# Kernel optimization log

Hardware: AMD Instinct MI355X
Metric: run time of the kernel (lower is better)

## Reference

```python
import jax, jax.numpy as jnp
import numpy as np

DIM = 4096
N_HEADS = 32
N_KV_HEADS = 8
HEAD_DIM = DIM // N_HEADS
N_REP = N_HEADS // N_KV_HEADS
SEQ_LEN = 2048
ROPE_THETA = 10000.0


def rope_cos_sin(head_dim, seq_len, theta):
    freqs = 1.0 / (theta ** (jnp.arange(0, head_dim, 2, dtype=jnp.float32) / head_dim))  # [hd/2]
    t = jnp.arange(seq_len, dtype=jnp.float32)
    angles = jnp.outer(t, freqs)  # [S, hd/2]
    return jnp.cos(angles), jnp.sin(angles)


def apply_rope(x, cos, sin):
    # x: [B, S, H, hd]; complex rotation on interleaved (even, odd) pairs
    xr = x[..., 0::2].astype(jnp.float32)
    xi = x[..., 1::2].astype(jnp.float32)
    c = cos[None, :, None, :]
    s = sin[None, :, None, :]
    out_r = xr * c - xi * s
    out_i = xr * s + xi * c
    out = jnp.stack([out_r, out_i], axis=-1).reshape(x.shape)
    return out.astype(x.dtype)


def setup_inputs() -> dict:
    key = jax.random.key(0)
    ks = jax.random.split(key, 5)
    x = jax.random.normal(ks[0], (1, SEQ_LEN, DIM), dtype=jnp.float32)
    wq = jax.random.normal(ks[1], (DIM, DIM), dtype=jnp.float32) * (DIM ** -0.5)
    wk = jax.random.normal(ks[2], (N_KV_HEADS * HEAD_DIM, DIM), dtype=jnp.float32) * (DIM ** -0.5)
    wv = jax.random.normal(ks[3], (N_KV_HEADS * HEAD_DIM, DIM), dtype=jnp.float32) * (DIM ** -0.5)
    wo = jax.random.normal(ks[4], (DIM, DIM), dtype=jnp.float32) * (DIM ** -0.5)
    return {"x": x, "start_pos": 0, "wq": wq, "wk": wk, "wv": wv, "wo": wo}


def reference(x, start_pos, wq, wk, wv, wo):
    bsz, seq_len, _ = x.shape
    # projections (torch Linear: y = x @ W.T)
    xq = (x @ wq.T).reshape(bsz, seq_len, N_HEADS, HEAD_DIM)
    xk = (x @ wk.T).reshape(bsz, seq_len, N_KV_HEADS, HEAD_DIM)
    xv = (x @ wv.T).reshape(bsz, seq_len, N_KV_HEADS, HEAD_DIM)

    cos, sin = rope_cos_sin(HEAD_DIM, seq_len, ROPE_THETA)
    xq = apply_rope(xq, cos, sin)
    xk = apply_rope(xk, cos, sin)

    # repeat_kv (GQA): [B, S, Hkv, hd] -> [B, S, Hkv*n_rep, hd]
    keys = jnp.repeat(xk, N_REP, axis=2)
    values = jnp.repeat(xv, N_REP, axis=2)

    # [B, H, S, hd]
    q = xq.transpose(0, 2, 1, 3)
    k = keys.transpose(0, 2, 1, 3)
    v = values.transpose(0, 2, 1, 3)

    scale = 1.0 / jnp.sqrt(jnp.asarray(HEAD_DIM, dtype=jnp.float32))
    scores = jnp.einsum('bhqd,bhkd->bhqk', q, k) * scale  # [B, H, S, S]
    causal = jnp.tril(jnp.ones((seq_len, seq_len), dtype=bool))
    scores = jnp.where(causal[None, None], scores, -jnp.inf)
    attn = jax.nn.softmax(scores.astype(jnp.float32), axis=-1).astype(q.dtype)
    out = jnp.einsum('bhqk,bhkd->bhqd', attn, v)  # [B, H, S, hd]
    out = out.transpose(0, 2, 1, 3).reshape(bsz, seq_len, -1)
    return out @ wo.T
```

## Files before the change

kernel.cpp:

```cpp
#include <hip/hip_runtime.h>

#define DIM 4096
#define KVDIM 1024
#define KVSTRIDE 2048
#define SEQ 2048
#define HEADS 32
#define HD 128

typedef __attribute__((ext_vector_type(8))) short bf16x8;
typedef __attribute__((ext_vector_type(4))) float f32x4;
typedef __attribute__((ext_vector_type(16))) float f32x16;
typedef __attribute__((ext_vector_type(4))) int int4v;

__device__ inline unsigned short f2bf(float f) {
    union { float f; unsigned int u; } v; v.f = f;
    unsigned int r = v.u + 0x7fffu + ((v.u >> 16) & 1u);
    return (unsigned short)(r >> 16);
}
__device__ inline float bf2f(unsigned short h) {
    union { unsigned int u; float f; } v; v.u = ((unsigned int)h) << 16;
    return v.f;
}

__device__ inline void gld16(const void* g, void* l) {
    __builtin_amdgcn_global_load_lds(
        (const __attribute__((address_space(1))) void*)g,
        (__attribute__((address_space(3))) void*)l, 16, 0, 0);
}

__device__ inline unsigned cvtpk(float a, float b) {
    unsigned r;
    asm("v_cvt_pk_bf16_f32 %0, %1, %2" : "=v"(r) : "v"(a), "v"(b));
    return r;
}

__global__ void convert_f32_bf16(const float* __restrict__ in,
                                 unsigned short* __restrict__ out, int n) {
    int i = (blockIdx.x * blockDim.x + threadIdx.x) * 8;
    if (i >= n) return;
    const float4* p = (const float4*)(in + i);
    float4 a = p[0], b = p[1];
    bf16x8 o;
    o[0] = (short)f2bf(a.x); o[1] = (short)f2bf(a.y);
    o[2] = (short)f2bf(a.z); o[3] = (short)f2bf(a.w);
    o[4] = (short)f2bf(b.x); o[5] = (short)f2bf(b.y);
    o[6] = (short)f2bf(b.z); o[7] = (short)f2bf(b.w);
    *(bf16x8*)(out + i) = o;
}

__global__ void rope_table(float* __restrict__ cs, float* __restrict__ sn) {
    int i = blockIdx.x * blockDim.x + threadIdx.x;
    if (i >= SEQ * 64) return;
    int m = i >> 6, f = i & 63;
    float freq = expf(-(float)f * (9.210340371976184f / 64.0f));
    float ang = (float)m * freq;
    float s, c;
    sincosf(ang, &s, &c);
    cs[i] = c; sn[i] = s;
}

__global__ void rope_apply(unsigned short* __restrict__ q, int lppr, int stride, float scale,
                           const float* __restrict__ cs, const float* __restrict__ sn) {
    int i = blockIdx.x * blockDim.x + threadIdx.x;
    int m = i >> lppr;
    int p = i & ((1 << lppr) - 1);
    if (m >= SEQ) return;
    int f = p & 63;
    int col = ((p >> 6) << 7) + (f << 1);
    size_t idx = (size_t)m * stride + col;
    unsigned int u = *(const unsigned int*)&q[idx];
    float xr = bf2f((unsigned short)(u & 0xffffu));
    float xi = bf2f((unsigned short)(u >> 16));
    float c = cs[(m << 6) + f], s = sn[(m << 6) + f];
    float orr = (xr * c - xi * s) * scale;
    float oi  = (xr * s + xi * c) * scale;
    unsigned int w = ((unsigned int)f2bf(oi) << 16) | (unsigned int)f2bf(orr);
    *(unsigned int*)&q[idx] = w;
}

template <bool OUT_BF16>
__global__ __launch_bounds__(256)
void gemm_bt(const unsigned short* __restrict__ A,
             const unsigned short* __restrict__ W,
             void* __restrict__ Cout, int M, int N, int K) {
    __shared__ __align__(16) unsigned short As[128 * 64];
    __shared__ __align__(16) unsigned short Ws[128 * 64];

    int nwg = gridDim.x * gridDim.y;
    int wg = blockIdx.y * gridDim.x + blockIdx.x;
    int cpx = nwg >> 3;
    wg = (wg & 7) * cpx + (wg >> 3);
    int bx = wg % gridDim.x, by = wg / gridDim.x;
    int brow = by * 128, bcol = bx * 128;

    int tid = threadIdx.x, lane = tid & 63, wid = tid >> 6;
    int wr = wid >> 1, wc = wid & 1, l15 = lane & 15, lq = lane >> 4;

    f32x4 acc[4][4] = {};

    for (int bk = 0; bk < K; bk += 64) {
        #pragma unroll
        for (int it = 0; it < 4; ++it) {
            int slot = it * 256 + wid * 64 + lane;
            int r = slot >> 3, g = slot & 7;
            gld16(&A[(size_t)(brow + r) * K + bk + ((g ^ (r & 7)) << 3)],
                  &As[(it * 256 + wid * 64) * 8]);
        }
        #pragma unroll
        for (int it = 0; it < 4; ++it) {
            int slot = it * 256 + wid * 64 + lane;
            int r = slot >> 3, g = slot & 7;
            gld16(&W[(size_t)(bcol + r) * K + bk + ((g ^ (r & 7)) << 3)],
                  &Ws[(it * 256 + wid * 64) * 8]);
        }
        __syncthreads();

        #pragma unroll
        for (int kk = 0; kk < 64; kk += 32) {
            int gb = (kk >> 3) + lq;
            bf16x8 af[4], bfr[4];
            #pragma unroll
            for (int m = 0; m < 4; ++m) {
                int r = wr * 64 + m * 16 + l15;
                af[m] = *(const bf16x8*)&As[r * 64 + ((gb ^ (r & 7)) << 3)];
            }
            #pragma unroll
            for (int n = 0; n < 4; ++n) {
                int r = wc * 64 + n * 16 + l15;
                bfr[n] = *(const bf16x8*)&Ws[r * 64 + ((gb ^ (r & 7)) << 3)];
            }
            #pragma unroll
            for (int m = 0; m < 4; ++m)
                #pragma unroll
                for (int n = 0; n < 4; ++n)
                    acc[m][n] = __builtin_amdgcn_mfma_f32_16x16x32_bf16(
                        af[m], bfr[n], acc[m][n], 0, 0, 0);
        }
        __syncthreads();
    }

    #pragma unroll
    for (int m = 0; m < 4; ++m) {
        #pragma unroll
        for (int n = 0; n < 4; ++n) {
            int row0 = brow + wr * 64 + m * 16 + lq * 4;
            int col = bcol + wc * 64 + n * 16 + l15;
            #pragma unroll
            for (int r = 0; r < 4; ++r) {
                if (OUT_BF16)
                    ((unsigned short*)Cout)[(size_t)(row0 + r) * N + col] = f2bf(acc[m][n][r]);
                else
                    ((float*)Cout)[(size_t)(row0 + r) * N + col] = acc[m][n][r];
            }
        }
    }
}

__global__ __launch_bounds__(256)
void attn_kernel(const unsigned short* __restrict__ Q,
                 const unsigned short* __restrict__ KV,
                 unsigned short* __restrict__ O) {
    __shared__ __align__(16) unsigned short ks[64 * 128];
    __shared__ __align__(16) unsigned short vt[128][66];

    int h = blockIdx.x;
    int yy = (gridDim.y - 1) - blockIdx.y;
    int q0 = yy * 128;
    int kvh = h >> 2;
    int tid = threadIdx.x, lane = tid & 63, wid = tid >> 6;
    int l31 = lane & 31, l5 = lane >> 5;
    int qw0 = q0 + wid * 32;

    bf16x8 qf[8];
    #pragma unroll
    for (int k8 = 0; k8 < 8; ++k8)
        qf[k8] = *(const bf16x8*)&Q[(size_t)(qw0 + l31) * DIM + h * HD + k8 * 16 + l5 * 8];

    f32x16 o_acc[4] = {};
    float m_run = -1e30f, l_run = 0.0f;

    int k4 = tid >> 4;
    int d0 = (tid & 15) * 8;

    int ntiles = (q0 + 128) >> 6;
    for (int t = 0; t < ntiles; ++t) {
        int kv0 = t * 64;
        #pragma unroll
        for (int it = 0; it < 4; ++it) {
            int slot = it * 256 + wid * 64 + lane;
            int r = slot >> 4, g = slot & 15;
            gld16(&KV[(size_t)(kv0 + r) * KVSTRIDE + kvh * HD + ((g ^ (r & 7)) << 3)],
                  &ks[(it * 256 + wid * 64) * 8]);
        }
        {
            bf16x8 v0 = *(const bf16x8*)&KV[(size_t)(kv0 + k4 * 4 + 0) * KVSTRIDE + KVDIM + kvh * HD + d0];
            bf16x8 v1 = *(const bf16x8*)&KV[(size_t)(kv0 + k4 * 4 + 1) * KVSTRIDE + KVDIM + kvh * HD + d0];
            bf16x8 v2 = *(const bf16x8*)&KV[(size_t)(kv0 + k4 * 4 + 2) * KVSTRIDE + KVDIM + kvh * HD + d0];
            bf16x8 v3 = *(const bf16x8*)&KV[(size_t)(kv0 + k4 * 4 + 3) * KVSTRIDE + KVDIM + kvh * HD + d0];
            #pragma unroll
            for (int j = 0; j < 8; ++j) {
                unsigned lo = ((unsigned)(unsigned short)v1[j] << 16) | (unsigned)(unsigned short)v0[j];
                unsigned hi = ((unsigned)(unsigned short)v3[j] << 16) | (unsigned)(unsigned short)v2[j];
                *(unsigned*)&vt[d0 + j][k4 * 4]     = lo;
                *(unsigned*)&vt[d0 + j][k4 * 4 + 2] = hi;
            }
        }
        __syncthreads();

        if (kv0 <= qw0 + 31) {
            #pragma unroll
            for (int sub = 0; sub < 2; ++sub) {
                int kvs = kv0 + sub * 32;
                if (kvs > qw0 + 31) continue;
                f32x16 s = {};
                #pragma unroll
                for (int k8 = 0; k8 < 8; ++k8) {
                    int r = sub * 32 + l31;
                    bf16x8 kf = *(const bf16x8*)&ks[r * 128 + (((k8 * 2 + l5) ^ (r & 7)) << 3)];
                    s = __builtin_amdgcn_mfma_f32_32x32x16_bf16(kf, qf[k8], s, 0, 0, 0);
                }
                if (kvs + 31 > qw0) {
                    #pragma unroll
                    for (int r = 0; r < 16; ++r) {
                        int kv = kvs + (r & 3) + ((r >> 2) << 3) + l5 * 4;
                        if (kv > qw0 + l31) s[r] = -1e30f;
                    }
                }
                float mx = s[0];
                #pragma unroll
                for (int r = 1; r < 16; ++r) mx = fmaxf(mx, s[r]);
                mx = fmaxf(mx, __shfl_xor(mx, 32));
                bool need = mx > m_run + 8.0f;
                if (__any((int)need)) {
                    float mn = fmaxf(m_run, mx);
                    float al = exp2f(m_run - mn);
                    m_run = mn;
                    l_run *= al;
                    #pragma unroll
                    for (int r = 0; r < 16; ++r) {
                        int qlr = (r & 3) + ((r >> 2) << 3) + l5 * 4;
                        float alO = __shfl(al, qlr, 32);
                        #pragma unroll
                        for (int t32 = 0; t32 < 4; ++t32) o_acc[t32][r] *= alO;
                    }
                }
                #pragma unroll
                for (int r = 0; r < 16; ++r) {
                    float p = exp2f(s[r] - m_run);
                    l_run += p;
                    s[r] = p;
                }
                bf16x8 pa[2];
                #pragma unroll
                for (int kk1 = 0; kk1 < 2; ++kk1) {
                    unsigned u0 = cvtpk(s[kk1 * 8 + 0], s[kk1 * 8 + 1]);
                    unsigned u1 = cvtpk(s[kk1 * 8 + 2], s[kk1 * 8 + 3]);
                    unsigned u2 = cvtpk(s[kk1 * 8 + 4], s[kk1 * 8 + 5]);
                    unsigned u3 = cvtpk(s[kk1 * 8 + 6], s[kk1 * 8 + 7]);
                    unsigned t0 = (unsigned)__shfl_xor((int)(l5 ? u0 : u2), 32);
                    unsigned t1 = (unsigned)__shfl_xor((int)(l5 ? u1 : u3), 32);
                    int4v w;
                    w.x = (int)(l5 ? t0 : u0);
                    w.y = (int)(l5 ? t1 : u1);
                    w.z = (int)(l5 ? u2 : t0);
                    w.w = (int)(l5 ? u3 : t1);
                    pa[kk1] = __builtin_bit_cast(bf16x8, w);
                }
                #pragma unroll
                for (int t32 = 0; t32 < 4; ++t32) {
                    #pragma unroll
                    for (int kk1 = 0; kk1 < 2; ++kk1) {
                        const unsigned short* vrow =
                            &vt[t32 * 32 + l31][sub * 32 + kk1 * 16 + l5 * 8];
                        int4v w;
                        w.x = *(const int*)&vrow[0];
                        w.y = *(const int*)&vrow[2];
                        w.z = *(const int*)&vrow[4];
                        w.w = *(const int*)&vrow[6];
                        o_acc[t32] = __builtin_amdgcn_mfma_f32_32x32x16_bf16(
                            pa[kk1], __builtin_bit_cast(bf16x8, w), o_acc[t32], 0, 0, 0);
                    }
                }
            }
        }
        __syncthreads();
    }

    float l_tot = l_run + __shfl_xor(l_run, 32);
    float rinv = __builtin_amdgcn_rcpf(l_tot);
    #pragma unroll
    for (int r = 0; r < 16; ++r) {
        int qlr = (r & 3) + ((r >> 2) << 3) + l5 * 4;
        float rl = __shfl(rinv, qlr, 32);
        #pragma unroll
        for (int t32 = 0; t32 < 4; ++t32)
            O[(size_t)(qw0 + qlr) * DIM + h * HD + t32 * 32 + l31] =
                f2bf(o_acc[t32][r] * rl);
    }
}

extern "C" void kernel_launch(void* const* d_in, const int* in_sizes, int n_in,
                              void* d_out, int out_size, void* d_ws, size_t ws_size,
                              hipStream_t stream) {
    const float* x  = (const float*)d_in[0];
    const float* wq = (const float*)d_in[2];
    const float* wk = (const float*)d_in[3];
    const float* wv = (const float*)d_in[4];
    const float* wo = (const float*)d_in[5];
    float* out = (float*)d_out;

    char* ws = (char*)d_ws;
    unsigned short* xb  = (unsigned short*)(ws);
    unsigned short* qb  = (unsigned short*)(ws + 16777216);
    unsigned short* kvb = (unsigned short*)(ws + 33554432);
    unsigned short* ab  = (unsigned short*)(ws + 41943040);
    float* cs = (float*)(ws + 58720256);
    float* sn = cs + SEQ * 64;
    unsigned short* wscratch = (unsigned short*)d_out;
    unsigned short* wob = (unsigned short*)(ws);

    const float SCALE2 = 0.08838834764831845f * 1.4426950408889634f;

    convert_f32_bf16<<<SEQ * DIM / 2048, 256, 0, stream>>>(x, xb, SEQ * DIM);
    rope_table<<<SEQ * 64 / 256, 256, 0, stream>>>(cs, sn);

    convert_f32_bf16<<<DIM * DIM / 2048, 256, 0, stream>>>(wq, wscratch, DIM * DIM);
    gemm_bt<true><<<dim3(DIM / 128, SEQ / 128), 256, 0, stream>>>(xb, wscratch, qb, SEQ, DIM, DIM);

    convert_f32_bf16<<<KVDIM * DIM / 2048, 256, 0, stream>>>(wk, wscratch, KVDIM * DIM);
    convert_f32_bf16<<<KVDIM * DIM / 2048, 256, 0, stream>>>(wv, wscratch + (size_t)KVDIM * DIM, KVDIM * DIM);
    gemm_bt<true><<<dim3(KVSTRIDE / 128, SEQ / 128), 256, 0, stream>>>(xb, wscratch, kvb, SEQ, KVSTRIDE, DIM);

    rope_apply<<<SEQ * (DIM / 2) / 256, 256, 0, stream>>>(qb, 11, DIM, SCALE2, cs, sn);
    rope_apply<<<SEQ * (KVDIM / 2) / 256, 256, 0, stream>>>(kvb, 9, KVSTRIDE, 1.0f, cs, sn);

    attn_kernel<<<dim3(HEADS, SEQ / 128), 256, 0, stream>>>(qb, kvb, ab);

    convert_f32_bf16<<<DIM * DIM / 2048, 256, 0, stream>>>(wo, wob, DIM * DIM);
    gemm_bt<false><<<dim3(DIM / 128, SEQ / 128), 256, 0, stream>>>(ab, wob, out, SEQ, DIM, DIM);
}
```

Before: 397.9 us.

## Split attention KV range across two wave groups and merge partial softmax

The attention kernel now runs 512 threads per block. Two groups of four waves each process alternating 64-row KV tiles for the same 128 query rows, and their partial max, sum and output are merged through shared memory at the end. The V transpose buffer now uses an XOR-swizzled layout so each MFMA operand is read with one 128-bit LDS load, and s_setprio is raised around the MFMA sections. The aim is more waves per CU and shorter serial KV loops. The cost is an extra merge step, a bf16 rounding of the partial output, and more LDS per block.

```diff
diff --git a/kernel.cpp b/kernel.cpp
--- a/kernel.cpp
+++ b/kernel.cpp
@@ -156,20 +156,77 @@
     }
 }
 
-__global__ __launch_bounds__(256)
+
+__device__ __forceinline__ void softmax_pack(
+    f32x16& s, f32x16* o_acc, float& m_run, float& l_run,
+    int qw0, int kvs, int l31, int l5, bf16x8* pa) {
+    if (kvs + 31 > qw0) {
+        #pragma unroll
+        for (int r = 0; r < 16; ++r) {
+            int kv = kvs + (r & 3) + ((r >> 2) << 3) + l5 * 4;
+            if (kv > qw0 + l31) s[r] = -1e30f;
+        }
+    }
+    float mx = s[0];
+    #pragma unroll
+    for (int r = 1; r < 16; ++r) mx = fmaxf(mx, s[r]);
+    mx = fmaxf(mx, __shfl_xor(mx, 32));
+    bool need = mx > m_run + 8.0f;
+    if (__any((int)need)) {
+        float mn = fmaxf(m_run, mx);
+        float al = exp2f(m_run - mn);
+        m_run = mn;
+        l_run *= al;
+        #pragma unroll
+        for (int r = 0; r < 16; ++r) {
+            int qlr = (r & 3) + ((r >> 2) << 3) + l5 * 4;
+            float alO = __shfl(al, qlr, 32);
+            #pragma unroll
+            for (int t32 = 0; t32 < 4; ++t32) o_acc[t32][r] *= alO;
+        }
+    }
+    #pragma unroll
+    for (int r = 0; r < 16; ++r) {
+        float p = exp2f(s[r] - m_run);
+        l_run += p;
+        s[r] = p;
+    }
+    #pragma unroll
+    for (int kk1 = 0; kk1 < 2; ++kk1) {
+        unsigned u0 = cvtpk(s[kk1 * 8 + 0], s[kk1 * 8 + 1]);
+        unsigned u1 = cvtpk(s[kk1 * 8 + 2], s[kk1 * 8 + 3]);
+        unsigned u2 = cvtpk(s[kk1 * 8 + 4], s[kk1 * 8 + 5]);
+        unsigned u3 = cvtpk(s[kk1 * 8 + 6], s[kk1 * 8 + 7]);
+        unsigned t0 = (unsigned)__shfl_xor((int)(l5 ? u0 : u2), 32);
+        unsigned t1 = (unsigned)__shfl_xor((int)(l5 ? u1 : u3), 32);
+        int4v w;
+        w.x = (int)(l5 ? t0 : u0);
+        w.y = (int)(l5 ? t1 : u1);
+        w.z = (int)(l5 ? u2 : t0);
+        w.w = (int)(l5 ? u3 : t1);
+        pa[kk1] = __builtin_bit_cast(bf16x8, w);
+    }
+}
+
+__global__ __launch_bounds__(512, 4)
 void attn_kernel(const unsigned short* __restrict__ Q,
                  const unsigned short* __restrict__ KV,
                  unsigned short* __restrict__ O) {
-    __shared__ __align__(16) unsigned short ks[64 * 128];
-    __shared__ __align__(16) unsigned short vt[128][66];
+    __shared__ __align__(16) unsigned short smem[32768];
+
+    unsigned short* ks0 = smem;
+    unsigned short* ks1 = smem + 8192;
+    unsigned short* vt0 = smem + 16384;
+    unsigned short* vt1 = smem + 24576;
 
     int h = blockIdx.x;
     int yy = (gridDim.y - 1) - blockIdx.y;
     int q0 = yy * 128;
     int kvh = h >> 2;
     int tid = threadIdx.x, lane = tid & 63, wid = tid >> 6;
+    int qsub = wid & 3, half = wid >> 2;
     int l31 = lane & 31, l5 = lane >> 5;
-    int qw0 = q0 + wid * 32;
+    int qw0 = q0 + qsub * 32;
 
     bf16x8 qf[8];
     #pragma unroll
@@ -179,123 +236,122 @@
     f32x16 o_acc[4] = {};
     float m_run = -1e30f, l_run = 0.0f;
 
-    int k4 = tid >> 4;
+    int k2 = tid >> 4;
     int d0 = (tid & 15) * 8;
-
-    int ntiles = (q0 + 128) >> 6;
-    for (int t = 0; t < ntiles; ++t) {
-        int kv0 = t * 64;
-        #pragma unroll
-        for (int it = 0; it < 4; ++it) {
-            int slot = it * 256 + wid * 64 + lane;
-            int r = slot >> 4, g = slot & 15;
-            gld16(&KV[(size_t)(kv0 + r) * KVSTRIDE + kvh * HD + ((g ^ (r & 7)) << 3)],
-                  &ks[(it * 256 + wid * 64) * 8]);
-        }
-        {
-            bf16x8 v0 = *(const bf16x8*)&KV[(size_t)(kv0 + k4 * 4 + 0) * KVSTRIDE + KVDIM + kvh * HD + d0];
-            bf16x8 v1 = *(const bf16x8*)&KV[(size_t)(kv0 + k4 * 4 + 1) * KVSTRIDE + KVDIM + kvh * HD + d0];
-            bf16x8 v2 = *(const bf16x8*)&KV[(size_t)(kv0 + k4 * 4 + 2) * KVSTRIDE + KVDIM + kvh * HD + d0];
-            bf16x8 v3 = *(const bf16x8*)&KV[(size_t)(kv0 + k4 * 4 + 3) * KVSTRIDE + KVDIM + kvh * HD + d0];
+    int vsub = (k2 & 3) * 2;
+    int vg = k2 >> 2;
+
+    const unsigned short* Kb = KV + kvh * HD;
+    const unsigned short* Vb = KV + KVDIM + kvh * HD;
+
+    unsigned short* myks = half ? ks1 : ks0;
+    unsigned short* myvt = half ? vt1 : vt0;
+
+    int np = yy + 1;
+    for (int i = 0; i < np; ++i) {
+        #pragma unroll
+        for (int tt = 0; tt < 2; ++tt) {
+            int kvb = (2 * i + tt) * 64;
+            unsigned short* kd = tt ? ks1 : ks0;
+            #pragma unroll
+            for (int it = 0; it < 2; ++it) {
+                int slot = it * 512 + tid;
+                int r = slot >> 4, g = slot & 15;
+                gld16(&Kb[(size_t)(kvb + r) * KVSTRIDE + ((g ^ (r & 7)) << 3)],
+                      &kd[(it * 512 + wid * 64) * 8]);
+            }
+        }
+        #pragma unroll
+        for (int tt = 0; tt < 2; ++tt) {
+            int kvb = (2 * i + tt) * 64;
+            unsigned short* vd = tt ? vt1 : vt0;
+            bf16x8 va = *(const bf16x8*)&Vb[(size_t)(kvb + k2 * 2) * KVSTRIDE + d0];
+            bf16x8 vb = *(const bf16x8*)&Vb[(size_t)(kvb + k2 * 2 + 1) * KVSTRIDE + d0];
             #pragma unroll
             for (int j = 0; j < 8; ++j) {
-                unsigned lo = ((unsigned)(unsigned short)v1[j] << 16) | (unsigned)(unsigned short)v0[j];
-                unsigned hi = ((unsigned)(unsigned short)v3[j] << 16) | (unsigned)(unsigned short)v2[j];
-                *(unsigned*)&vt[d0 + j][k4 * 4]     = lo;
-                *(unsigned*)&vt[d0 + j][k4 * 4 + 2] = hi;
+                int row = d0 + j;
+                int swz = ((row >> 3) ^ row) & 7;
+                unsigned w = ((unsigned)(unsigned short)vb[j] << 16) |
+                             (unsigned)(unsigned short)va[j];
+                *(unsigned*)&vd[row * 64 + ((vg ^ swz) << 3) + vsub] = w;
             }
         }
         __syncthreads();
 
+        int kv0 = (2 * i + half) * 64;
         if (kv0 <= qw0 + 31) {
             #pragma unroll
             for (int sub = 0; sub < 2; ++sub) {
                 int kvs = kv0 + sub * 32;
                 if (kvs > qw0 + 31) continue;
                 f32x16 s = {};
+                __builtin_amdgcn_s_setprio(1);
                 #pragma unroll
                 for (int k8 = 0; k8 < 8; ++k8) {
                     int r = sub * 32 + l31;
-                    bf16x8 kf = *(const bf16x8*)&ks[r * 128 + (((k8 * 2 + l5) ^ (r & 7)) << 3)];
+                    bf16x8 kf = *(const bf16x8*)&myks[r * 128 + (((k8 * 2 + l5) ^ (r & 7)) << 3)];
                     s = __builtin_amdgcn_mfma_f32_32x32x16_bf16(kf, qf[k8], s, 0, 0, 0);
                 }
-                if (kvs + 31 > qw0) {
-                    #pragma unroll
-                    for (int r = 0; r < 16; ++r) {
-                        int kv = kvs + (r & 3) + ((r >> 2) << 3) + l5 * 4;
-                        if (kv > qw0 + l31) s[r] = -1e30f;
-                    }
-                }
-                float mx = s[0];
-                #pragma unroll
-                for (int r = 1; r < 16; ++r) mx = fmaxf(mx, s[r]);
-                mx = fmaxf(mx, __shfl_xor(mx, 32));
-                bool need = mx > m_run + 8.0f;
-                if (__any((int)need)) {
-                    float mn = fmaxf(m_run, mx);
-                    float al = exp2f(m_run - mn);
-                    m_run = mn;
-                    l_run *= al;
-                    #pragma unroll
-                    for (int r = 0; r < 16; ++r) {
-                        int qlr = (r & 3) + ((r >> 2) << 3) + l5 * 4;
-                        float alO = __shfl(al, qlr, 32);
-                        #pragma unroll
-                        for (int t32 = 0; t32 < 4; ++t32) o_acc[t32][r] *= alO;
-                    }
-                }
-                #pragma unroll
-                for (int r = 0; r < 16; ++r) {
-                    float p = exp2f(s[r] - m_run);
-                    l_run += p;
-                    s[r] = p;
-                }
+                __builtin_amdgcn_s_setprio(0);
                 bf16x8 pa[2];
-                #pragma unroll
-                for (int kk1 = 0; kk1 < 2; ++kk1) {
-                    unsigned u0 = cvtpk(s[kk1 * 8 + 0], s[kk1 * 8 + 1]);
-                    unsigned u1 = cvtpk(s[kk1 * 8 + 2], s[kk1 * 8 + 3]);
-                    unsigned u2 = cvtpk(s[kk1 * 8 + 4], s[kk1 * 8 + 5]);
-                    unsigned u3 = cvtpk(s[kk1 * 8 + 6], s[kk1 * 8 + 7]);
-                    unsigned t0 = (unsigned)__shfl_xor((int)(l5 ? u0 : u2), 32);
-                    unsigned t1 = (unsigned)__shfl_xor((int)(l5 ? u1 : u3), 32);
-                    int4v w;
-                    w.x = (int)(l5 ? t0 : u0);
-                    w.y = (int)(l5 ? t1 : u1);
-                    w.z = (int)(l5 ? u2 : t0);
-                    w.w = (int)(l5 ? u3 : t1);
-                    pa[kk1] = __builtin_bit_cast(bf16x8, w);
-                }
+                softmax_pack(s, o_acc, m_run, l_run, qw0, kvs, l31, l5, pa);
+                __builtin_amdgcn_s_setprio(1);
                 #pragma unroll
                 for (int t32 = 0; t32 < 4; ++t32) {
+                    int d = t32 * 32 + l31;
+                    int swz = ((d >> 3) ^ d) & 7;
                     #pragma unroll
                     for (int kk1 = 0; kk1 < 2; ++kk1) {
-                        const unsigned short* vrow =
-                            &vt[t32 * 32 + l31][sub * 32 + kk1 * 16 + l5 * 8];
-                        int4v w;
-                        w.x = *(const int*)&vrow[0];
-                        w.y = *(const int*)&vrow[2];
-                        w.z = *(const int*)&vrow[4];
-                        w.w = *(const int*)&vrow[6];
+                        int g = sub * 4 + kk1 * 2 + l5;
+                        int4v w = *(const int4v*)&myvt[d * 64 + ((g ^ swz) << 3)];
                         o_acc[t32] = __builtin_amdgcn_mfma_f32_32x32x16_bf16(
                             pa[kk1], __builtin_bit_cast(bf16x8, w), o_acc[t32], 0, 0, 0);
                     }
                 }
+                __builtin_amdgcn_s_setprio(0);
             }
         }
         __syncthreads();
     }
 
-    float l_tot = l_run + __shfl_xor(l_run, 32);
-    float rinv = __builtin_amdgcn_rcpf(l_tot);
-    #pragma unroll
-    for (int r = 0; r < 16; ++r) {
-        int qlr = (r & 3) + ((r >> 2) << 3) + l5 * 4;
-        float rl = __shfl(rinv, qlr, 32);
-        #pragma unroll
-        for (int t32 = 0; t32 < 4; ++t32)
-            O[(size_t)(qw0 + qlr) * DIM + h * HD + t32 * 32 + l31] =
-                f2bf(o_acc[t32][r] * rl);
+    float* part_m = (float*)smem;
+    float* part_l = (float*)(smem + 512);
+    unsigned* part_o = (unsigned*)(smem + 1024);
+
+    if (half == 1) {
+        part_m[qsub * 64 + lane] = m_run;
+        part_l[qsub * 64 + lane] = l_run;
+        #pragma unroll
+        for (int t32 = 0; t32 < 4; ++t32) {
+            unsigned* po = &part_o[((qsub * 4 + t32) * 64 + lane) * 8];
+            #pragma unroll
+            for (int p = 0; p < 8; ++p)
+                po[p] = cvtpk(o_acc[t32][2 * p], o_acc[t32][2 * p + 1]);
+        }
+    }
+    __syncthreads();
+    if (half == 0) {
+        float m1 = part_m[qsub * 64 + lane];
+        float l1 = part_l[qsub * 64 + lane];
+        float mm = fmaxf(m_run, m1);
+        float a0 = exp2f(m_run - mm), a1 = exp2f(m1 - mm);
+        float lm = l_run * a0 + l1 * a1;
+        float l_tot = lm + __shfl_xor(lm, 32);
+        float rinv = __builtin_amdgcn_rcpf(l_tot);
+        #pragma unroll
+        for (int r = 0; r < 16; ++r) {
+            int qlr = (r & 3) + ((r >> 2) << 3) + l5 * 4;
+            float A0 = __shfl(a0, qlr, 32);
+            float A1 = __shfl(a1, qlr, 32);
+            float rl = __shfl(rinv, qlr, 32);
+            #pragma unroll
+            for (int t32 = 0; t32 < 4; ++t32) {
+                unsigned u = part_o[((qsub * 4 + t32) * 64 + lane) * 8 + (r >> 1)];
+                float o1 = bf2f((unsigned short)((r & 1) ? (u >> 16) : (u & 0xffffu)));
+                float om = o_acc[t32][r] * A0 + o1 * A1;
+                O[(size_t)(qw0 + qlr) * DIM + h * HD + t32 * 32 + l31] = f2bf(om * rl);
+            }
+        }
     }
 }
 
@@ -334,7 +390,7 @@
     rope_apply<<<SEQ * (DIM / 2) / 256, 256, 0, stream>>>(qb, 11, DIM, SCALE2, cs, sn);
     rope_apply<<<SEQ * (KVDIM / 2) / 256, 256, 0, stream>>>(kvb, 9, KVSTRIDE, 1.0f, cs, sn);
 
-    attn_kernel<<<dim3(HEADS, SEQ / 128), 256, 0, stream>>>(qb, kvb, ab);
+    attn_kernel<<<dim3(HEADS, 16), 512, 0, stream>>>(qb, kvb, ab);
 
     convert_f32_bf16<<<DIM * DIM / 2048, 256, 0, stream>>>(wo, wob, DIM * DIM);
     gemm_bt<false><<<dim3(DIM / 128, SEQ / 128), 256, 0, stream>>>(ab, wob, out, SEQ, DIM, DIM);
```

Result: slower. 469.4 us (+18.0%).

## Split causal attention KV range in two halves and merge partial results

Applied to the files above, without the earlier changes.

The attention grid doubles so that each 128-query block's KV tiles are split evenly between two workgroups. This targets the causal load imbalance and the low block count of the previous launch. Each half writes an unnormalized bf16 partial output plus per-row max and sum, and a new merge kernel rescales and combines them. The change also swizzles the transposed V layout in LDS so each read is a single 16-byte access, adds s_setprio around the MFMA sections, and sets a launch-bounds occupancy hint. The cost is an extra kernel pass over the output and extra rounding from storing unnormalized partials in bf16.

```diff
diff --git a/kernel.cpp b/kernel.cpp
--- a/kernel.cpp
+++ b/kernel.cpp
@@ -156,15 +156,71 @@
     }
 }
 
-__global__ __launch_bounds__(256)
+
+__device__ __forceinline__ void softmax_pack(
+    f32x16& s, f32x16* o_acc, float& m_run, float& l_run,
+    int qw0, int kvs, int l31, int l5, bf16x8* pa) {
+    if (kvs + 31 > qw0) {
+        #pragma unroll
+        for (int r = 0; r < 16; ++r) {
+            int kv = kvs + (r & 3) + ((r >> 2) << 3) + l5 * 4;
+            if (kv > qw0 + l31) s[r] = -1e30f;
+        }
+    }
+    float mx = s[0];
+    #pragma unroll
+    for (int r = 1; r < 16; ++r) mx = fmaxf(mx, s[r]);
+    mx = fmaxf(mx, __shfl_xor(mx, 32));
+    bool need = mx > m_run + 8.0f;
+    if (__any((int)need)) {
+        float mn = fmaxf(m_run, mx);
+        float al = exp2f(m_run - mn);
+        m_run = mn;
+        l_run *= al;
+        #pragma unroll
+        for (int r = 0; r < 16; ++r) {
+            int qlr = (r & 3) + ((r >> 2) << 3) + l5 * 4;
+            float alO = __shfl(al, qlr, 32);
+            #pragma unroll
+            for (int t32 = 0; t32 < 4; ++t32) o_acc[t32][r] *= alO;
+        }
+    }
+    #pragma unroll
+    for (int r = 0; r < 16; ++r) {
+        float p = exp2f(s[r] - m_run);
+        l_run += p;
+        s[r] = p;
+    }
+    #pragma unroll
+    for (int kk1 = 0; kk1 < 2; ++kk1) {
+        unsigned u0 = cvtpk(s[kk1 * 8 + 0], s[kk1 * 8 + 1]);
+        unsigned u1 = cvtpk(s[kk1 * 8 + 2], s[kk1 * 8 + 3]);
+        unsigned u2 = cvtpk(s[kk1 * 8 + 4], s[kk1 * 8 + 5]);
+        unsigned u3 = cvtpk(s[kk1 * 8 + 6], s[kk1 * 8 + 7]);
+        unsigned t0 = (unsigned)__shfl_xor((int)(l5 ? u0 : u2), 32);
+        unsigned t1 = (unsigned)__shfl_xor((int)(l5 ? u1 : u3), 32);
+        int4v w;
+        w.x = (int)(l5 ? t0 : u0);
+        w.y = (int)(l5 ? t1 : u1);
+        w.z = (int)(l5 ? u2 : t0);
+        w.w = (int)(l5 ? u3 : t1);
+        pa[kk1] = __builtin_bit_cast(bf16x8, w);
+    }
+}
+
+__global__ __launch_bounds__(256, 4)
 void attn_kernel(const unsigned short* __restrict__ Q,
                  const unsigned short* __restrict__ KV,
-                 unsigned short* __restrict__ O) {
+                 unsigned short* __restrict__ pO0,
+                 unsigned short* __restrict__ pO1,
+                 float2* __restrict__ ml) {
     __shared__ __align__(16) unsigned short ks[64 * 128];
-    __shared__ __align__(16) unsigned short vt[128][66];
+    __shared__ __align__(16) unsigned short vt[128 * 64];
 
     int h = blockIdx.x;
-    int yy = (gridDim.y - 1) - blockIdx.y;
+    int by = blockIdx.y;
+    int yy = 15 - (by >> 1);
+    int half = by & 1;
     int q0 = yy * 128;
     int kvh = h >> 2;
     int tid = threadIdx.x, lane = tid & 63, wid = tid >> 6;
@@ -181,28 +237,33 @@
 
     int k4 = tid >> 4;
     int d0 = (tid & 15) * 8;
-
-    int ntiles = (q0 + 128) >> 6;
-    for (int t = 0; t < ntiles; ++t) {
+    int vsub = (k4 & 1) * 4;
+    int vg = k4 >> 1;
+
+    const unsigned short* Kb = KV + kvh * HD;
+    const unsigned short* Vb = KV + KVDIM + kvh * HD;
+
+    int t0 = half * (yy + 1), t1 = t0 + (yy + 1);
+    for (int t = t0; t < t1; ++t) {
         int kv0 = t * 64;
         #pragma unroll
         for (int it = 0; it < 4; ++it) {
             int slot = it * 256 + wid * 64 + lane;
             int r = slot >> 4, g = slot & 15;
-            gld16(&KV[(size_t)(kv0 + r) * KVSTRIDE + kvh * HD + ((g ^ (r & 7)) << 3)],
+            gld16(&Kb[(size_t)(kv0 + r) * KVSTRIDE + ((g ^ (r & 7)) << 3)],
                   &ks[(it * 256 + wid * 64) * 8]);
         }
-        {
-            bf16x8 v0 = *(const bf16x8*)&KV[(size_t)(kv0 + k4 * 4 + 0) * KVSTRIDE + KVDIM + kvh * HD + d0];
-            bf16x8 v1 = *(const bf16x8*)&KV[(size_t)(kv0 + k4 * 4 + 1) * KVSTRIDE + KVDIM + kvh * HD + d0];
-            bf16x8 v2 = *(const bf16x8*)&KV[(size_t)(kv0 + k4 * 4 + 2) * KVSTRIDE + KVDIM + kvh * HD + d0];
-            bf16x8 v3 = *(const bf16x8*)&KV[(size_t)(kv0 + k4 * 4 + 3) * KVSTRIDE + KVDIM + kvh * HD + d0];
+        #pragma unroll
+        for (int pass = 0; pass < 2; ++pass) {
+            bf16x8 va = *(const bf16x8*)&Vb[(size_t)(kv0 + k4 * 4 + pass * 2) * KVSTRIDE + d0];
+            bf16x8 vb = *(const bf16x8*)&Vb[(size_t)(kv0 + k4 * 4 + pass * 2 + 1) * KVSTRIDE + d0];
             #pragma unroll
             for (int j = 0; j < 8; ++j) {
-                unsigned lo = ((unsigned)(unsigned short)v1[j] << 16) | (unsigned)(unsigned short)v0[j];
-                unsigned hi = ((unsigned)(unsigned short)v3[j] << 16) | (unsigned)(unsigned short)v2[j];
-                *(unsigned*)&vt[d0 + j][k4 * 4]     = lo;
-                *(unsigned*)&vt[d0 + j][k4 * 4 + 2] = hi;
+                int row = d0 + j;
+                int swz = ((row >> 3) ^ row) & 7;
+                unsigned w = ((unsigned)(unsigned short)vb[j] << 16) |
+                             (unsigned)(unsigned short)va[j];
+                *(unsigned*)&vt[row * 64 + ((vg ^ swz) << 3) + vsub + pass * 2] = w;
             }
         }
         __syncthreads();
@@ -213,90 +274,72 @@
                 int kvs = kv0 + sub * 32;
                 if (kvs > qw0 + 31) continue;
                 f32x16 s = {};
+                __builtin_amdgcn_s_setprio(1);
                 #pragma unroll
                 for (int k8 = 0; k8 < 8; ++k8) {
                     int r = sub * 32 + l31;
                     bf16x8 kf = *(const bf16x8*)&ks[r * 128 + (((k8 * 2 + l5) ^ (r & 7)) << 3)];
                     s = __builtin_amdgcn_mfma_f32_32x32x16_bf16(kf, qf[k8], s, 0, 0, 0);
                 }
-                if (kvs + 31 > qw0) {
-                    #pragma unroll
-                    for (int r = 0; r < 16; ++r) {
-                        int kv = kvs + (r & 3) + ((r >> 2) << 3) + l5 * 4;
-                        if (kv > qw0 + l31) s[r] = -1e30f;
-                    }
-                }
-                float mx = s[0];
-                #pragma unroll
-                for (int r = 1; r < 16; ++r) mx = fmaxf(mx, s[r]);
-                mx = fmaxf(mx, __shfl_xor(mx, 32));
-                bool need = mx > m_run + 8.0f;
-                if (__any((int)need)) {
-                    float mn = fmaxf(m_run, mx);
-                    float al = exp2f(m_run - mn);
-                    m_run = mn;
-                    l_run *= al;
-                    #pragma unroll
-                    for (int r = 0; r < 16; ++r) {
-                        int qlr = (r & 3) + ((r >> 2) << 3) + l5 * 4;
-                        float alO = __shfl(al, qlr, 32);
-                        #pragma unroll
-                        for (int t32 = 0; t32 < 4; ++t32) o_acc[t32][r] *= alO;
-                    }
-                }
-                #pragma unroll
-                for (int r = 0; r < 16; ++r) {
-                    float p = exp2f(s[r] - m_run);
-                    l_run += p;
-                    s[r] = p;
-                }
+                __builtin_amdgcn_s_setprio(0);
                 bf16x8 pa[2];
-                #pragma unroll
-                for (int kk1 = 0; kk1 < 2; ++kk1) {
-                    unsigned u0 = cvtpk(s[kk1 * 8 + 0], s[kk1 * 8 + 1]);
-                    unsigned u1 = cvtpk(s[kk1 * 8 + 2], s[kk1 * 8 + 3]);
-                    unsigned u2 = cvtpk(s[kk1 * 8 + 4], s[kk1 * 8 + 5]);
-                    unsigned u3 = cvtpk(s[kk1 * 8 + 6], s[kk1 * 8 + 7]);
-                    unsigned t0 = (unsigned)__shfl_xor((int)(l5 ? u0 : u2), 32);
-                    unsigned t1 = (unsigned)__shfl_xor((int)(l5 ? u1 : u3), 32);
-                    int4v w;
-                    w.x = (int)(l5 ? t0 : u0);
-                    w.y = (int)(l5 ? t1 : u1);
-                    w.z = (int)(l5 ? u2 : t0);
-                    w.w = (int)(l5 ? u3 : t1);
-                    pa[kk1] = __builtin_bit_cast(bf16x8, w);
-                }
+                softmax_pack(s, o_acc, m_run, l_run, qw0, kvs, l31, l5, pa);
+                __builtin_amdgcn_s_setprio(1);
                 #pragma unroll
                 for (int t32 = 0; t32 < 4; ++t32) {
+                    int d = t32 * 32 + l31;
+                    int swz = ((d >> 3) ^ d) & 7;
                     #pragma unroll
                     for (int kk1 = 0; kk1 < 2; ++kk1) {
-                        const unsigned short* vrow =
-                            &vt[t32 * 32 + l31][sub * 32 + kk1 * 16 + l5 * 8];
-                        int4v w;
-                        w.x = *(const int*)&vrow[0];
-                        w.y = *(const int*)&vrow[2];
-                        w.z = *(const int*)&vrow[4];
-                        w.w = *(const int*)&vrow[6];
+                        int g = sub * 4 + kk1 * 2 + l5;
+                        int4v w = *(const int4v*)&vt[d * 64 + ((g ^ swz) << 3)];
                         o_acc[t32] = __builtin_amdgcn_mfma_f32_32x32x16_bf16(
                             pa[kk1], __builtin_bit_cast(bf16x8, w), o_acc[t32], 0, 0, 0);
                     }
                 }
+                __builtin_amdgcn_s_setprio(0);
             }
         }
         __syncthreads();
     }
 
-    float l_tot = l_run + __shfl_xor(l_run, 32);
-    float rinv = __builtin_amdgcn_rcpf(l_tot);
+    float l_half = l_run + __shfl_xor(l_run, 32);
+    if (l5 == 0) {
+        float2 v; v.x = m_run; v.y = l_half;
+        ml[((size_t)(half << 11) + qw0 + l31) * 32 + h] = v;
+    }
+    unsigned short* pO = half ? pO1 : pO0;
     #pragma unroll
     for (int r = 0; r < 16; ++r) {
         int qlr = (r & 3) + ((r >> 2) << 3) + l5 * 4;
-        float rl = __shfl(rinv, qlr, 32);
         #pragma unroll
         for (int t32 = 0; t32 < 4; ++t32)
-            O[(size_t)(qw0 + qlr) * DIM + h * HD + t32 * 32 + l31] =
-                f2bf(o_acc[t32][r] * rl);
-    }
+            pO[(size_t)(qw0 + qlr) * DIM + h * HD + t32 * 32 + l31] =
+                f2bf(o_acc[t32][r]);
+    }
+}
+
+__global__ void attn_merge(const unsigned short* __restrict__ pO0,
+                           unsigned short* __restrict__ pO1out,
+                           const float2* __restrict__ ml) {
+    int i = blockIdx.x * blockDim.x + threadIdx.x;
+    int base = i * 8;
+    if (base >= SEQ * DIM) return;
+    int row = base >> 12;
+    int h = (base & 4095) >> 7;
+    float2 ml0 = ml[(size_t)row * 32 + h];
+    float2 ml1 = ml[(size_t)(2048 + row) * 32 + h];
+    float mm = fmaxf(ml0.x, ml1.x);
+    float a0 = exp2f(ml0.x - mm), a1 = exp2f(ml1.x - mm);
+    float rinv = __builtin_amdgcn_rcpf(ml0.y * a0 + ml1.y * a1);
+    bf16x8 o0 = *(const bf16x8*)&pO0[base];
+    bf16x8 o1 = *(const bf16x8*)&pO1out[base];
+    bf16x8 o;
+    #pragma unroll
+    for (int j = 0; j < 8; ++j)
+        o[j] = (short)f2bf((bf2f((unsigned short)o0[j]) * a0 +
+                            bf2f((unsigned short)o1[j]) * a1) * rinv);
+    *(bf16x8*)&pO1out[base] = o;
 }
 
 extern "C" void kernel_launch(void* const* d_in, const int* in_sizes, int n_in,
@@ -316,6 +359,7 @@
     unsigned short* ab  = (unsigned short*)(ws + 41943040);
     float* cs = (float*)(ws + 58720256);
     float* sn = cs + SEQ * 64;
+    float2* ml = (float2*)(ws + 58720256);
     unsigned short* wscratch = (unsigned short*)d_out;
     unsigned short* wob = (unsigned short*)(ws);
 
@@ -334,7 +378,8 @@
     rope_apply<<<SEQ * (DIM / 2) / 256, 256, 0, stream>>>(qb, 11, DIM, SCALE2, cs, sn);
     rope_apply<<<SEQ * (KVDIM / 2) / 256, 256, 0, stream>>>(kvb, 9, KVSTRIDE, 1.0f, cs, sn);
 
-    attn_kernel<<<dim3(HEADS, SEQ / 128), 256, 0, stream>>>(qb, kvb, ab);
+    attn_kernel<<<dim3(HEADS, 32), 256, 0, stream>>>(qb, kvb, xb, ab, ml);
+    attn_merge<<<SEQ * DIM / 8 / 256, 256, 0, stream>>>(xb, ab, ml);
 
     convert_f32_bf16<<<DIM * DIM / 2048, 256, 0, stream>>>(wo, wob, DIM * DIM);
     gemm_bt<false><<<dim3(DIM / 128, SEQ / 128), 256, 0, stream>>>(ab, wob, out, SEQ, DIM, DIM);
```

Result: slower. 550.4 us (+38.3%).

## Fuse Q and KV projections into one GEMM with RoPE in epilogue

Applied to the files above, without the earlier changes.

Merges the separate Q and KV projection GEMMs into a single launch over a 48x16 grid, where column blocks select the Q or KV weight. RoPE and the softmax scale are applied in the GEMM epilogue using a lane shuffle to pair even and odd columns, which removes the two rope_apply passes over Q and K. The fused launch should also fill the GPU better than two separate grids did. In exchange, the epilogue does extra table loads and shuffles, and the KV weights are staged in the attention output buffer.

```diff
diff --git a/kernel.cpp b/kernel.cpp
--- a/kernel.cpp
+++ b/kernel.cpp
@@ -6,6 +6,7 @@
 #define SEQ 2048
 #define HEADS 32
 #define HD 128
+#define SCALE2F 0.12753785016058262f
 
 typedef __attribute__((ext_vector_type(8))) short bf16x8;
 typedef __attribute__((ext_vector_type(4))) float f32x4;
@@ -59,25 +60,6 @@
     cs[i] = c; sn[i] = s;
 }
 
-__global__ void rope_apply(unsigned short* __restrict__ q, int lppr, int stride, float scale,
-                           const float* __restrict__ cs, const float* __restrict__ sn) {
-    int i = blockIdx.x * blockDim.x + threadIdx.x;
-    int m = i >> lppr;
-    int p = i & ((1 << lppr) - 1);
-    if (m >= SEQ) return;
-    int f = p & 63;
-    int col = ((p >> 6) << 7) + (f << 1);
-    size_t idx = (size_t)m * stride + col;
-    unsigned int u = *(const unsigned int*)&q[idx];
-    float xr = bf2f((unsigned short)(u & 0xffffu));
-    float xi = bf2f((unsigned short)(u >> 16));
-    float c = cs[(m << 6) + f], s = sn[(m << 6) + f];
-    float orr = (xr * c - xi * s) * scale;
-    float oi  = (xr * s + xi * c) * scale;
-    unsigned int w = ((unsigned int)f2bf(oi) << 16) | (unsigned int)f2bf(orr);
-    *(unsigned int*)&q[idx] = w;
-}
-
 template <bool OUT_BF16>
 __global__ __launch_bounds__(256)
 void gemm_bt(const unsigned short* __restrict__ A,
@@ -151,6 +133,105 @@
                     ((unsigned short*)Cout)[(size_t)(row0 + r) * N + col] = f2bf(acc[m][n][r]);
                 else
                     ((float*)Cout)[(size_t)(row0 + r) * N + col] = acc[m][n][r];
+            }
+        }
+    }
+}
+
+__global__ __launch_bounds__(256)
+void gemm_qkv(const unsigned short* __restrict__ A,
+              const unsigned short* __restrict__ Wq,
+              const unsigned short* __restrict__ Wkv,
+              unsigned short* __restrict__ Qout,
+              unsigned short* __restrict__ KVout,
+              const float* __restrict__ cs, const float* __restrict__ sn) {
+    __shared__ __align__(16) unsigned short As[128 * 64];
+    __shared__ __align__(16) unsigned short Ws[128 * 64];
+    const int K = DIM;
+
+    int nwg = gridDim.x * gridDim.y;
+    int wg = blockIdx.y * gridDim.x + blockIdx.x;
+    int cpx = nwg >> 3;
+    wg = (wg & 7) * cpx + (wg >> 3);
+    int bx = wg % gridDim.x, by = wg / gridDim.x;
+    int brow = by * 128, bcol = bx * 128;
+
+    bool isQ = bx < 32;
+    const unsigned short* Wb = isQ ? Wq : Wkv;
+    int wrow0 = isQ ? bcol : bcol - 4096;
+
+    int tid = threadIdx.x, lane = tid & 63, wid = tid >> 6;
+    int wr = wid >> 1, wc = wid & 1, l15 = lane & 15, lq = lane >> 4;
+
+    f32x4 acc[4][4] = {};
+
+    for (int bk = 0; bk < K; bk += 64) {
+        #pragma unroll
+        for (int it = 0; it < 4; ++it) {
+            int slot = it * 256 + wid * 64 + lane;
+            int r = slot >> 3, g = slot & 7;
+            gld16(&A[(size_t)(brow + r) * K + bk + ((g ^ (r & 7)) << 3)],
+                  &As[(it * 256 + wid * 64) * 8]);
+        }
+        #pragma unroll
+        for (int it = 0; it < 4; ++it) {
+            int slot = it * 256 + wid * 64 + lane;
+            int r = slot >> 3, g = slot & 7;
+            gld16(&Wb[(size_t)(wrow0 + r) * K + bk + ((g ^ (r & 7)) << 3)],
+                  &Ws[(it * 256 + wid * 64) * 8]);
+        }
+        __syncthreads();
+
+        #pragma unroll
+        for (int kk = 0; kk < 64; kk += 32) {
+            int gb = (kk >> 3) + lq;
+            bf16x8 af[4], bfr[4];
+            #pragma unroll
+            for (int m = 0; m < 4; ++m) {
+                int r = wr * 64 + m * 16 + l15;
+                af[m] = *(const bf16x8*)&As[r * 64 + ((gb ^ (r & 7)) << 3)];
+            }
+            #pragma unroll
+            for (int n = 0; n < 4; ++n) {
+                int r = wc * 64 + n * 16 + l15;
+                bfr[n] = *(const bf16x8*)&Ws[r * 64 + ((gb ^ (r & 7)) << 3)];
+            }
+            #pragma unroll
+            for (int m = 0; m < 4; ++m)
+                #pragma unroll
+                for (int n = 0; n < 4; ++n)
+                    acc[m][n] = __builtin_amdgcn_mfma_f32_16x16x32_bf16(
+                        af[m], bfr[n], acc[m][n], 0, 0, 0);
+        }
+        __syncthreads();
+    }
+
+    bool dorope = bx < 40;
+    float scl = isQ ? SCALE2F : 1.0f;
+    unsigned short* outp = isQ ? Qout : KVout;
+    int ostride = isQ ? DIM : KVSTRIDE;
+    int ocol0 = wrow0 + wc * 64;
+    bool evenlane = (l15 & 1) == 0;
+
+    #pragma unroll
+    for (int m = 0; m < 4; ++m) {
+        #pragma unroll
+        for (int n = 0; n < 4; ++n) {
+            int col = ocol0 + n * 16 + l15;
+            int f = (col & 127) >> 1;
+            int row0 = brow + wr * 64 + m * 16 + lq * 4;
+            #pragma unroll
+            for (int r = 0; r < 4; ++r) {
+                float v = acc[m][n][r];
+                if (dorope) {
+                    float p = __shfl_xor(v, 1);
+                    int ti = ((row0 + r) << 6) + f;
+                    float c = cs[ti], s = sn[ti];
+                    float xr = evenlane ? v : p;
+                    float xi = evenlane ? p : v;
+                    v = (evenlane ? (xr * c - xi * s) : (xr * s + xi * c)) * scl;
+                }
+                outp[(size_t)(row0 + r) * ostride + col] = f2bf(v);
             }
         }
     }
@@ -310,29 +391,24 @@
     float* out = (float*)d_out;
 
     char* ws = (char*)d_ws;
-    unsigned short* xb  = (unsigned short*)(ws);
-    unsigned short* qb  = (unsigned short*)(ws + 16777216);
-    unsigned short* kvb = (unsigned short*)(ws + 33554432);
-    unsigned short* ab  = (unsigned short*)(ws + 41943040);
+    unsigned short* xb   = (unsigned short*)(ws);
+    unsigned short* qb   = (unsigned short*)(ws + 16777216);
+    unsigned short* kvb  = (unsigned short*)(ws + 33554432);
+    unsigned short* ab   = (unsigned short*)(ws + 41943040);
     float* cs = (float*)(ws + 58720256);
     float* sn = cs + SEQ * 64;
-    unsigned short* wscratch = (unsigned short*)d_out;
-    unsigned short* wob = (unsigned short*)(ws);
-
-    const float SCALE2 = 0.08838834764831845f * 1.4426950408889634f;
+    unsigned short* wqb  = (unsigned short*)d_out;
+    unsigned short* wkvb = ab;
+    unsigned short* wob  = (unsigned short*)(ws);
 
     convert_f32_bf16<<<SEQ * DIM / 2048, 256, 0, stream>>>(x, xb, SEQ * DIM);
     rope_table<<<SEQ * 64 / 256, 256, 0, stream>>>(cs, sn);
 
-    convert_f32_bf16<<<DIM * DIM / 2048, 256, 0, stream>>>(wq, wscratch, DIM * DIM);
-    gemm_bt<true><<<dim3(DIM / 128, SEQ / 128), 256, 0, stream>>>(xb, wscratch, qb, SEQ, DIM, DIM);
-
-    convert_f32_bf16<<<KVDIM * DIM / 2048, 256, 0, stream>>>(wk, wscratch, KVDIM * DIM);
-    convert_f32_bf16<<<KVDIM * DIM / 2048, 256, 0, stream>>>(wv, wscratch + (size_t)KVDIM * DIM, KVDIM * DIM);
-    gemm_bt<true><<<dim3(KVSTRIDE / 128, SEQ / 128), 256, 0, stream>>>(xb, wscratch, kvb, SEQ, KVSTRIDE, DIM);
-
-    rope_apply<<<SEQ * (DIM / 2) / 256, 256, 0, stream>>>(qb, 11, DIM, SCALE2, cs, sn);
-    rope_apply<<<SEQ * (KVDIM / 2) / 256, 256, 0, stream>>>(kvb, 9, KVSTRIDE, 1.0f, cs, sn);
+    convert_f32_bf16<<<DIM * DIM / 2048, 256, 0, stream>>>(wq, wqb, DIM * DIM);
+    convert_f32_bf16<<<KVDIM * DIM / 2048, 256, 0, stream>>>(wk, wkvb, KVDIM * DIM);
+    convert_f32_bf16<<<KVDIM * DIM / 2048, 256, 0, stream>>>(wv, wkvb + (size_t)KVDIM * DIM, KVDIM * DIM);
+
+    gemm_qkv<<<dim3(48, 16), 256, 0, stream>>>(xb, wqb, wkvb, qb, kvb, cs, sn);
 
     attn_kernel<<<dim3(HEADS, SEQ / 128), 256, 0, stream>>>(qb, kvb, ab);
 
```

Result: no change. 405.7 us (+1.9%).
